# Optimization experiments

Hardware: AMD Instinct MI355X
Metric: run time of the kernel (lower is better)

The kernel has to match this reference:

```python
import jax, jax.numpy as jnp
import numpy as np
from jax.ops import segment_sum

N_NODES = 100000


def _deg_inv_sqrt(idx, n):
    # DGL GraphConv norm='both': degs clamped to min 1, then deg^{-0.5}
    deg = segment_sum(jnp.ones_like(idx, dtype=jnp.float32), idx, num_segments=n)
    return jnp.where(deg > 0, jax.lax.rsqrt(jnp.maximum(deg, 1.0)), 1.0)


def _graph_conv(x, src, dst, W, b, out_norm, in_norm, n):
    # norm='both': scale src feats by out_deg^-1/2, sum-aggregate, scale by in_deg^-1/2
    h = (x * out_norm[:, None]) @ W          # apply weight first (cheaper/equal width)
    msg = h[src]                              # [E, d] irregular gather
    agg = segment_sum(msg, dst, num_segments=n)
    return agg * in_norm[:, None] + b


def setup_inputs() -> dict:
    key = jax.random.key(0)
    k1, k2, k3, k4, k5, k6, k7 = jax.random.split(key, 7)
    E = 1600000
    in_feats, h_feats, out_feats = 128, 128, 64
    in_feat = jax.random.normal(k1, (N_NODES, in_feats), dtype=jnp.float32)
    src = jax.random.randint(k2, (E,), 0, N_NODES, dtype=jnp.int32)
    dst = jax.random.randint(k3, (E,), 0, N_NODES, dtype=jnp.int32)
    # Glorot-style init like dgl GraphConv
    W1 = jax.random.normal(k4, (in_feats, h_feats), dtype=jnp.float32) * (1.0 / np.sqrt(in_feats))
    b1 = jnp.zeros((h_feats,), dtype=jnp.float32)
    W2 = jax.random.normal(k5, (h_feats, out_feats), dtype=jnp.float32) * (1.0 / np.sqrt(h_feats))
    b2 = jnp.zeros((out_feats,), dtype=jnp.float32)
    return {"in_feat": in_feat, "src": src, "dst": dst, "W1": W1, "b1": b1, "W2": W2, "b2": b2}


def reference(in_feat, src, dst, W1, b1, W2, b2):
    n = in_feat.shape[0]
    out_norm = _deg_inv_sqrt(src, n)  # out-degree norm (source side)
    in_norm = _deg_inv_sqrt(dst, n)   # in-degree norm (destination side)
    h = _graph_conv(in_feat, src, dst, W1, b1, out_norm, in_norm, n)
    z = jax.nn.relu(h)
    h2 = _graph_conv(z, src, dst, W2, b2, out_norm, in_norm, n)
    return (h2, z)
```

## Files before the change

### kernel.cpp

```cpp
#include <hip/hip_runtime.h>

#define N_NODES 100000
#define N_EDGES 1600000
#define NB 391
#define BCAP 5120
#define PART_BLOCKS 250
#define EPB 6400
#define GSTRIDE 16

typedef __attribute__((ext_vector_type(8))) short short8;
typedef __attribute__((ext_vector_type(4))) float f32x4;

__device__ inline unsigned short f2bf(float f) {
    unsigned int u = __builtin_bit_cast(unsigned int, f);
    u += 0x7fffu + ((u >> 16) & 1u);
    return (unsigned short)(u >> 16);
}
__device__ inline float bf2f(unsigned short h) {
    unsigned int u = ((unsigned int)h) << 16;
    return __builtin_bit_cast(float, u);
}

__global__ __launch_bounds__(256) void k_part(const int* __restrict__ src, const int* __restrict__ dst,
                                              int* __restrict__ gcurD, int* __restrict__ gcurS,
                                              unsigned int* __restrict__ ebuf,
                                              unsigned char* __restrict__ ebufS,
                                              const float* __restrict__ W1, const float* __restrict__ W2,
                                              unsigned short* __restrict__ Wp1, unsigned short* __restrict__ Wp2) {
    if (blockIdx.x >= PART_BLOCKS) {
        int i = (blockIdx.x - PART_BLOCKS) * 256 + threadIdx.x;
        if (i < 2048) {
            int kq = i >> 7, c = i & 127;
#pragma unroll
            for (int j = 0; j < 8; j++) Wp1[i * 8 + j] = f2bf(W1[(kq * 8 + j) * 128 + c]);
        } else if (i < 3072) {
            int i2 = i - 2048;
            int kq = i2 >> 6, c = i2 & 63;
#pragma unroll
            for (int j = 0; j < 8; j++) Wp2[i2 * 8 + j] = f2bf(W2[(kq * 8 + j) * 64 + c]);
        }
        return;
    }
    __shared__ int histD[NB], gbaseD[NB];
    __shared__ int histS[NB], gbaseS[NB];
    for (int i = threadIdx.x; i < NB; i += 256) { histD[i] = 0; histS[i] = 0; }
    __syncthreads();
    int base = blockIdx.x * EPB;
    for (int i = threadIdx.x; i < EPB; i += 256) {
        int d = dst[base + i], s = src[base + i];
        atomicAdd(&histD[d >> 8], 1);
        atomicAdd(&histS[s >> 8], 1);
    }
    __syncthreads();
    for (int i = threadIdx.x; i < NB; i += 256) {
        int hD = histD[i], hS = histS[i];
        gbaseD[i] = hD ? atomicAdd(&gcurD[i * GSTRIDE], hD) : 0;
        gbaseS[i] = hS ? atomicAdd(&gcurS[i * GSTRIDE], hS) : 0;
        histD[i] = 0;
        histS[i] = 0;
    }
    __syncthreads();
    for (int i = threadIdx.x; i < EPB; i += 256) {
        int d = dst[base + i], s = src[base + i];
        int bd = d >> 8;
        int r = atomicAdd(&histD[bd], 1);
        int pos = gbaseD[bd] + r;
        if (pos < BCAP) ebuf[(size_t)bd * BCAP + pos] = ((unsigned int)s << 8) | (unsigned int)(d & 255);
        int bs = s >> 8;
        int r2 = atomicAdd(&histS[bs], 1);
        int pos2 = gbaseS[bs] + r2;
        if (pos2 < BCAP) ebufS[(size_t)bs * BCAP + pos2] = (unsigned char)(s & 255);
    }
}

__global__ __launch_bounds__(256) void k_bhist_scan(const unsigned char* __restrict__ ebufS,
                                                    const int* __restrict__ gcurS,
                                                    float* __restrict__ out_norm,
                                                    const int* __restrict__ gcurD,
                                                    int* __restrict__ bbase, int* __restrict__ row_ptr) {
    int t = threadIdx.x;
    if (blockIdx.x < NB) {
        __shared__ int hist[256];
        int b = blockIdx.x;
        hist[t] = 0;
        __syncthreads();
        int ne = min(gcurS[b * GSTRIDE], BCAP);
        const unsigned char* eb = ebufS + (size_t)b * BCAP;
        int nv = ne >> 2;
        const uchar4* ev = (const uchar4*)eb;
        for (int i = t; i < nv; i += 256) {
            uchar4 u = ev[i];
            atomicAdd(&hist[u.x], 1); atomicAdd(&hist[u.y], 1);
            atomicAdd(&hist[u.z], 1); atomicAdd(&hist[u.w], 1);
        }
        for (int i = (nv << 2) + t; i < ne; i += 256) atomicAdd(&hist[eb[i]], 1);
        __syncthreads();
        int node = b * 256 + t;
        if (node < N_NODES) out_norm[node] = hist[t] > 0 ? rsqrtf((float)hist[t]) : 1.0f;
    } else {
        __shared__ int s[NB + 1];
        for (int i = t; i < NB; i += 256) s[i] = min(gcurD[i * GSTRIDE], BCAP);
        __syncthreads();
        if (t == 0) {
            int run = 0;
            for (int b = 0; b < NB; b++) { int v = s[b]; s[b] = run; run += v; }
            s[NB] = run;
        }
        __syncthreads();
        for (int i = t; i < NB + 1; i += 256) bbase[i] = s[i];
        if (t == 0) row_ptr[N_NODES] = s[NB];
    }
}

__global__ __launch_bounds__(256) void k_bsort_xb(const unsigned int* __restrict__ ebuf, const int* __restrict__ gcurD,
                                                  const int* __restrict__ bbase, int* __restrict__ csr_src,
                                                  int* __restrict__ row_ptr, float* __restrict__ in_norm,
                                                  const float* __restrict__ x, const float* __restrict__ out_norm,
                                                  unsigned short* __restrict__ xb) {
    __shared__ int perm[BCAP];
    __shared__ int hist[256], cursor[256], sa[256], sb[256];
    int t = threadIdx.x;
    if (blockIdx.x >= NB) {
        int tid = (blockIdx.x - NB) * 256 + t;
        int row = tid >> 5;
        float4 v = ((const float4*)x)[tid];
        float w = out_norm[row];
        unsigned int lo = (unsigned int)f2bf(v.x * w) | ((unsigned int)f2bf(v.y * w) << 16);
        unsigned int hi = (unsigned int)f2bf(v.z * w) | ((unsigned int)f2bf(v.w * w) << 16);
        ((uint2*)xb)[tid] = make_uint2(lo, hi);
        return;
    }
    int b = blockIdx.x;
    int ne = min(gcurD[b * GSTRIDE], BCAP);
    const unsigned int* eb = ebuf + (size_t)b * BCAP;
    hist[t] = 0;
    __syncthreads();
    for (int i = t; i < ne; i += 256) atomicAdd(&hist[eb[i] & 255u], 1);
    __syncthreads();
    sa[t] = hist[t];
    __syncthreads();
    int* cur = sa; int* nxt = sb;
    for (int o = 1; o < 256; o <<= 1) {
        int v = cur[t] + (t >= o ? cur[t - o] : 0);
        nxt[t] = v;
        __syncthreads();
        int* tmp = cur; cur = nxt; nxt = tmp;
    }
    int ex = cur[t] - hist[t];
    cursor[t] = ex;
    int node = b * 256 + t;
    if (node < N_NODES) {
        row_ptr[node] = bbase[b] + ex;
        in_norm[node] = hist[t] > 0 ? rsqrtf((float)hist[t]) : 1.0f;
    }
    __syncthreads();
    for (int i = t; i < ne; i += 256) {
        unsigned int pk = eb[i];
        int pos = atomicAdd(&cursor[pk & 255u], 1);
        perm[pos] = (int)(pk >> 8);
    }
    __syncthreads();
    int gb = bbase[b];
    for (int i = t; i < ne; i += 256) csr_src[gb + i] = perm[i];
}

__global__ __launch_bounds__(256) void k_agg1(const unsigned short* __restrict__ xb,
                                              const int* __restrict__ row_ptr, const int* __restrict__ csr,
                                              const float* __restrict__ in_norm,
                                              unsigned short* __restrict__ aggb) {
    int wave = threadIdx.x >> 6, lane = threadIdx.x & 63;
    int d = blockIdx.x * 4 + wave;
    if (d >= N_NODES) return;
    int e0 = __builtin_amdgcn_readfirstlane(row_ptr[d]);
    int e1 = __builtin_amdgcn_readfirstlane(row_ptr[d + 1]);
    int col = lane << 1;
    float accL[8], accH[8];
#pragma unroll
    for (int j = 0; j < 8; j++) { accL[j] = 0.f; accH[j] = 0.f; }
    int e = e0;
    for (; e + 8 <= e1; e += 8) {
        int sI[8];
#pragma unroll
        for (int j = 0; j < 8; j++) sI[j] = __builtin_amdgcn_readfirstlane(csr[e + j]);
        unsigned int v[8];
#pragma unroll
        for (int j = 0; j < 8; j++) v[j] = *(const unsigned int*)(xb + (size_t)sI[j] * 128 + col);
#pragma unroll
        for (int j = 0; j < 8; j++) {
            accL[j] += bf2f((unsigned short)(v[j] & 0xffffu));
            accH[j] += bf2f((unsigned short)(v[j] >> 16));
        }
    }
    if (e + 4 <= e1) {
        int sI[4];
#pragma unroll
        for (int j = 0; j < 4; j++) sI[j] = __builtin_amdgcn_readfirstlane(csr[e + j]);
        unsigned int v[4];
#pragma unroll
        for (int j = 0; j < 4; j++) v[j] = *(const unsigned int*)(xb + (size_t)sI[j] * 128 + col);
#pragma unroll
        for (int j = 0; j < 4; j++) {
            accL[j] += bf2f((unsigned short)(v[j] & 0xffffu));
            accH[j] += bf2f((unsigned short)(v[j] >> 16));
        }
        e += 4;
    }
    if (e + 2 <= e1) {
        int sI[2];
#pragma unroll
        for (int j = 0; j < 2; j++) sI[j] = __builtin_amdgcn_readfirstlane(csr[e + j]);
        unsigned int v[2];
#pragma unroll
        for (int j = 0; j < 2; j++) v[j] = *(const unsigned int*)(xb + (size_t)sI[j] * 128 + col);
#pragma unroll
        for (int j = 0; j < 2; j++) {
            accL[j] += bf2f((unsigned short)(v[j] & 0xffffu));
            accH[j] += bf2f((unsigned short)(v[j] >> 16));
        }
        e += 2;
    }
    if (e < e1) {
        int s = __builtin_amdgcn_readfirstlane(csr[e]);
        unsigned int v = *(const unsigned int*)(xb + (size_t)s * 128 + col);
        accL[0] += bf2f((unsigned short)(v & 0xffffu));
        accH[0] += bf2f((unsigned short)(v >> 16));
    }
    float a0 = 0.f, a1 = 0.f;
#pragma unroll
    for (int j = 0; j < 8; j++) { a0 += accL[j]; a1 += accH[j]; }
    float w = in_norm[d];
    unsigned int pk = (unsigned int)f2bf(a0 * w) | ((unsigned int)f2bf(a1 * w) << 16);
    *(unsigned int*)(aggb + (size_t)d * 128 + col) = pk;
}

__global__ __launch_bounds__(256) void k_gemm12(const unsigned short* __restrict__ Ab,
                                                const unsigned short* __restrict__ Wp1,
                                                const unsigned short* __restrict__ Wp2,
                                                const float* __restrict__ bias1,
                                                const float* __restrict__ out_norm,
                                                float* __restrict__ z_out,
                                                unsigned short* __restrict__ tb) {
    __shared__ __align__(16) unsigned short lds1[16 * 128 * 8];
    __shared__ __align__(16) unsigned short lds2[16 * 64 * 8];
    __shared__ __align__(16) unsigned short zt[64 * 132];
    {
        const uint4* s1 = (const uint4*)Wp1; uint4* d1 = (uint4*)lds1;
        for (int i = threadIdx.x; i < 2048; i += 256) d1[i] = s1[i];
        const uint4* s2 = (const uint4*)Wp2; uint4* d2 = (uint4*)lds2;
        for (int i = threadIdx.x; i < 1024; i += 256) d2[i] = s2[i];
    }
    __syncthreads();
    int wave = threadIdx.x >> 6, lane = threadIdx.x & 63;
    int base = (blockIdx.x * 4 + wave) * 16;
    if (base >= N_NODES) return;
    int m = lane & 15, q = lane >> 4;
    short8 a[4];
#pragma unroll
    for (int t = 0; t < 4; t++) a[t] = *(const short8*)(Ab + (size_t)(base + m) * 128 + t * 32 + q * 8);
    f32x4 acc[8];
#pragma unroll
    for (int c = 0; c < 8; c++) acc[c] = (f32x4)(0.f);
#pragma unroll
    for (int ct = 0; ct < 8; ct++) {
#pragma unroll
        for (int t = 0; t < 4; t++) {
            short8 b = *(const short8*)(lds1 + ((t * 4 + q) * 128 + ct * 16 + m) * 8);
            acc[ct] = __builtin_amdgcn_mfma_f32_16x16x32_bf16(a[t], b, acc[ct], 0, 0, 0);
        }
    }
    float onr[4];
#pragma unroll
    for (int i = 0; i < 4; i++) onr[i] = out_norm[base + q * 4 + i];
#pragma unroll
    for (int ct = 0; ct < 8; ct++) {
        int col = ct * 16 + m;
        float bv = bias1[col];
#pragma unroll
        for (int i = 0; i < 4; i++) {
            int row = base + q * 4 + i;
            float v = acc[ct][i] + bv;
            v = v > 0.f ? v : 0.f;
            z_out[(size_t)row * 128 + col] = v;
            zt[(wave * 16 + q * 4 + i) * 132 + col] = f2bf(v * onr[i]);
        }
    }
    short8 a2[4];
#pragma unroll
    for (int t = 0; t < 4; t++) a2[t] = *(const short8*)(zt + (wave * 16 + m) * 132 + t * 32 + q * 8);
    f32x4 acc2[4];
#pragma unroll
    for (int c = 0; c < 4; c++) acc2[c] = (f32x4)(0.f);
#pragma unroll
    for (int ct = 0; ct < 4; ct++) {
#pragma unroll
        for (int t = 0; t < 4; t++) {
            short8 b = *(const short8*)(lds2 + ((t * 4 + q) * 64 + ct * 16 + m) * 8);
            acc2[ct] = __builtin_amdgcn_mfma_f32_16x16x32_bf16(a2[t], b, acc2[ct], 0, 0, 0);
        }
    }
#pragma unroll
    for (int ct = 0; ct < 4; ct++) {
        int col = ct * 16 + m;
#pragma unroll
        for (int i = 0; i < 4; i++) {
            int row = base + q * 4 + i;
            tb[(size_t)row * 64 + col] = f2bf(acc2[ct][i]);
        }
    }
}

__global__ __launch_bounds__(256) void k_agg2(const unsigned short* __restrict__ tb,
                                              const int* __restrict__ row_ptr, const int* __restrict__ csr,
                                              const float* __restrict__ in_norm, const float* __restrict__ b2,
                                              float* __restrict__ out_h2) {
    int wave = threadIdx.x >> 6, lane = threadIdx.x & 63;
    int d = blockIdx.x * 4 + wave;
    if (d >= N_NODES) return;
    int e0 = __builtin_amdgcn_readfirstlane(row_ptr[d]);
    int e1 = __builtin_amdgcn_readfirstlane(row_ptr[d + 1]);
    float acc[8];
#pragma unroll
    for (int j = 0; j < 8; j++) acc[j] = 0.f;
    int e = e0;
    for (; e + 8 <= e1; e += 8) {
        int sI[8];
#pragma unroll
        for (int j = 0; j < 8; j++) sI[j] = __builtin_amdgcn_readfirstlane(csr[e + j]);
        unsigned short v[8];
#pragma unroll
        for (int j = 0; j < 8; j++) v[j] = tb[(size_t)sI[j] * 64 + lane];
#pragma unroll
        for (int j = 0; j < 8; j++) acc[j] += bf2f(v[j]);
    }
    if (e + 4 <= e1) {
        int sI[4];
#pragma unroll
        for (int j = 0; j < 4; j++) sI[j] = __builtin_amdgcn_readfirstlane(csr[e + j]);
        unsigned short v[4];
#pragma unroll
        for (int j = 0; j < 4; j++) v[j] = tb[(size_t)sI[j] * 64 + lane];
#pragma unroll
        for (int j = 0; j < 4; j++) acc[j] += bf2f(v[j]);
        e += 4;
    }
    if (e + 2 <= e1) {
        int sI[2];
#pragma unroll
        for (int j = 0; j < 2; j++) sI[j] = __builtin_amdgcn_readfirstlane(csr[e + j]);
        unsigned short v[2];
#pragma unroll
        for (int j = 0; j < 2; j++) v[j] = tb[(size_t)sI[j] * 64 + lane];
#pragma unroll
        for (int j = 0; j < 2; j++) acc[j] += bf2f(v[j]);
        e += 2;
    }
    if (e < e1) {
        int s = __builtin_amdgcn_readfirstlane(csr[e]);
        acc[0] += bf2f(tb[(size_t)s * 64 + lane]);
    }
    float a = 0.f;
#pragma unroll
    for (int j = 0; j < 8; j++) a += acc[j];
    out_h2[(size_t)d * 64 + lane] = a * in_norm[d] + b2[lane];
}

extern "C" void kernel_launch(void* const* d_in, const int* in_sizes, int n_in,
                              void* d_out, int out_size, void* d_ws, size_t ws_size,
                              hipStream_t stream) {
    const float* x   = (const float*)d_in[0];
    const int*   src = (const int*)d_in[1];
    const int*   dst = (const int*)d_in[2];
    const float* W1  = (const float*)d_in[3];
    const float* b1  = (const float*)d_in[4];
    const float* W2  = (const float*)d_in[5];
    const float* b2  = (const float*)d_in[6];
    float* out_h2 = (float*)d_out;
    float* out_z  = (float*)d_out + N_NODES * 64;

    char* ws = (char*)d_ws;
    size_t off = 0;
    auto alloc = [&](size_t bytes) -> char* {
        char* p = ws + off;
        off = (off + bytes + 255) & ~(size_t)255;
        return p;
    };
    int* gcurD    = (int*)alloc(NB * GSTRIDE * 4);
    int* gcurS    = (int*)alloc(NB * GSTRIDE * 4);
    int* bbase    = (int*)alloc((NB + 1) * 4);
    int* row_ptr  = (int*)alloc((N_NODES + 1) * 4);
    float* out_norm = (float*)alloc(N_NODES * 4);
    float* in_norm  = (float*)alloc(N_NODES * 4);
    unsigned int* ebuf = (unsigned int*)alloc((size_t)NB * BCAP * 4);
    unsigned char* ebufS = (unsigned char*)alloc((size_t)NB * BCAP);
    int* csr_src  = (int*)alloc((size_t)N_EDGES * 4);
    unsigned short* Wp1 = (unsigned short*)alloc(2048 * 8 * 2);
    unsigned short* Wp2 = (unsigned short*)alloc(1024 * 8 * 2);
    unsigned short* xb    = (unsigned short*)alloc((size_t)N_NODES * 128 * 2);
    unsigned short* agg1b = (unsigned short*)alloc((size_t)N_NODES * 128 * 2);
    unsigned short* tb    = (unsigned short*)alloc((size_t)N_NODES * 64 * 2);
    (void)ws_size; (void)in_sizes; (void)n_in; (void)out_size;

    hipMemsetAsync(gcurD, 0, NB * GSTRIDE * 4, stream);
    hipMemsetAsync(gcurS, 0, NB * GSTRIDE * 4, stream);

    const int GD_AGG = (N_NODES + 3) / 4;
    const int GD_GEMM = (N_NODES / 16 + 3) / 4;
    const int GD_XB = N_NODES * 32 / 256;

    k_part<<<PART_BLOCKS + 12, 256, 0, stream>>>(src, dst, gcurD, gcurS, ebuf, ebufS, W1, W2, Wp1, Wp2);
    k_bhist_scan<<<NB + 1, 256, 0, stream>>>(ebufS, gcurS, out_norm, gcurD, bbase, row_ptr);
    k_bsort_xb<<<NB + GD_XB, 256, 0, stream>>>(ebuf, gcurD, bbase, csr_src, row_ptr, in_norm, x, out_norm, xb);
    k_agg1<<<GD_AGG, 256, 0, stream>>>(xb, row_ptr, csr_src, in_norm, agg1b);
    k_gemm12<<<GD_GEMM, 256, 0, stream>>>(agg1b, Wp1, Wp2, b1, out_norm, out_z, tb);
    k_agg2<<<GD_AGG, 256, 0, stream>>>(tb, row_ptr, csr_src, in_norm, b2, out_h2);
}
```

Baseline: 300.8 us.

## Replace source-bucket histogram with global atomic degree counts and drop scan kernel

Source out-degrees are now counted with global atomics into a per-node array. This replaces the second bucketing pass into a byte buffer and its per-bucket histogram kernel. The bucket-base prefix scan is folded into the sort kernel, where each block sums the preceding bucket counts itself, so one kernel launch and the byte buffer disappear. The partition kernel also moves to 1024-thread blocks, the two memsets merge into one, and consumers compute rsqrt of the degree inline. The cost is 1.6M contended global atomics and a redundant per-block reduction over up to 391 counts.

```diff
diff --git a/kernel.cpp b/kernel.cpp
--- a/kernel.cpp
+++ b/kernel.cpp
@@ -21,14 +21,13 @@
     return __builtin_bit_cast(float, u);
 }
 
-__global__ __launch_bounds__(256) void k_part(const int* __restrict__ src, const int* __restrict__ dst,
-                                              int* __restrict__ gcurD, int* __restrict__ gcurS,
-                                              unsigned int* __restrict__ ebuf,
-                                              unsigned char* __restrict__ ebufS,
-                                              const float* __restrict__ W1, const float* __restrict__ W2,
-                                              unsigned short* __restrict__ Wp1, unsigned short* __restrict__ Wp2) {
+__global__ __launch_bounds__(1024) void k_part(const int* __restrict__ src, const int* __restrict__ dst,
+                                               int* __restrict__ gcurD, int* __restrict__ degS,
+                                               unsigned int* __restrict__ ebuf,
+                                               const float* __restrict__ W1, const float* __restrict__ W2,
+                                               unsigned short* __restrict__ Wp1, unsigned short* __restrict__ Wp2) {
     if (blockIdx.x >= PART_BLOCKS) {
-        int i = (blockIdx.x - PART_BLOCKS) * 256 + threadIdx.x;
+        int i = (blockIdx.x - PART_BLOCKS) * 1024 + threadIdx.x;
         if (i < 2048) {
             int kq = i >> 7, c = i & 127;
 #pragma unroll
@@ -42,80 +41,35 @@
         return;
     }
     __shared__ int histD[NB], gbaseD[NB];
-    __shared__ int histS[NB], gbaseS[NB];
-    for (int i = threadIdx.x; i < NB; i += 256) { histD[i] = 0; histS[i] = 0; }
+    int t = threadIdx.x;
+    for (int i = t; i < NB; i += 1024) histD[i] = 0;
     __syncthreads();
     int base = blockIdx.x * EPB;
-    for (int i = threadIdx.x; i < EPB; i += 256) {
+    for (int i = t; i < EPB; i += 1024) {
         int d = dst[base + i], s = src[base + i];
         atomicAdd(&histD[d >> 8], 1);
-        atomicAdd(&histS[s >> 8], 1);
-    }
-    __syncthreads();
-    for (int i = threadIdx.x; i < NB; i += 256) {
-        int hD = histD[i], hS = histS[i];
-        gbaseD[i] = hD ? atomicAdd(&gcurD[i * GSTRIDE], hD) : 0;
-        gbaseS[i] = hS ? atomicAdd(&gcurS[i * GSTRIDE], hS) : 0;
+        atomicAdd(&degS[s], 1);
+    }
+    __syncthreads();
+    for (int i = t; i < NB; i += 1024) {
+        int h = histD[i];
+        gbaseD[i] = h ? atomicAdd(&gcurD[i * GSTRIDE], h) : 0;
         histD[i] = 0;
-        histS[i] = 0;
-    }
-    __syncthreads();
-    for (int i = threadIdx.x; i < EPB; i += 256) {
+    }
+    __syncthreads();
+    for (int i = t; i < EPB; i += 1024) {
         int d = dst[base + i], s = src[base + i];
         int bd = d >> 8;
         int r = atomicAdd(&histD[bd], 1);
         int pos = gbaseD[bd] + r;
         if (pos < BCAP) ebuf[(size_t)bd * BCAP + pos] = ((unsigned int)s << 8) | (unsigned int)(d & 255);
-        int bs = s >> 8;
-        int r2 = atomicAdd(&histS[bs], 1);
-        int pos2 = gbaseS[bs] + r2;
-        if (pos2 < BCAP) ebufS[(size_t)bs * BCAP + pos2] = (unsigned char)(s & 255);
-    }
-}
-
-__global__ __launch_bounds__(256) void k_bhist_scan(const unsigned char* __restrict__ ebufS,
-                                                    const int* __restrict__ gcurS,
-                                                    float* __restrict__ out_norm,
-                                                    const int* __restrict__ gcurD,
-                                                    int* __restrict__ bbase, int* __restrict__ row_ptr) {
-    int t = threadIdx.x;
-    if (blockIdx.x < NB) {
-        __shared__ int hist[256];
-        int b = blockIdx.x;
-        hist[t] = 0;
-        __syncthreads();
-        int ne = min(gcurS[b * GSTRIDE], BCAP);
-        const unsigned char* eb = ebufS + (size_t)b * BCAP;
-        int nv = ne >> 2;
-        const uchar4* ev = (const uchar4*)eb;
-        for (int i = t; i < nv; i += 256) {
-            uchar4 u = ev[i];
-            atomicAdd(&hist[u.x], 1); atomicAdd(&hist[u.y], 1);
-            atomicAdd(&hist[u.z], 1); atomicAdd(&hist[u.w], 1);
-        }
-        for (int i = (nv << 2) + t; i < ne; i += 256) atomicAdd(&hist[eb[i]], 1);
-        __syncthreads();
-        int node = b * 256 + t;
-        if (node < N_NODES) out_norm[node] = hist[t] > 0 ? rsqrtf((float)hist[t]) : 1.0f;
-    } else {
-        __shared__ int s[NB + 1];
-        for (int i = t; i < NB; i += 256) s[i] = min(gcurD[i * GSTRIDE], BCAP);
-        __syncthreads();
-        if (t == 0) {
-            int run = 0;
-            for (int b = 0; b < NB; b++) { int v = s[b]; s[b] = run; run += v; }
-            s[NB] = run;
-        }
-        __syncthreads();
-        for (int i = t; i < NB + 1; i += 256) bbase[i] = s[i];
-        if (t == 0) row_ptr[N_NODES] = s[NB];
     }
 }
 
 __global__ __launch_bounds__(256) void k_bsort_xb(const unsigned int* __restrict__ ebuf, const int* __restrict__ gcurD,
-                                                  const int* __restrict__ bbase, int* __restrict__ csr_src,
+                                                  int* __restrict__ csr_src,
                                                   int* __restrict__ row_ptr, float* __restrict__ in_norm,
-                                                  const float* __restrict__ x, const float* __restrict__ out_norm,
+                                                  const float* __restrict__ x, const int* __restrict__ degS,
                                                   unsigned short* __restrict__ xb) {
     __shared__ int perm[BCAP];
     __shared__ int hist[256], cursor[256], sa[256], sb[256];
@@ -124,7 +78,8 @@
         int tid = (blockIdx.x - NB) * 256 + t;
         int row = tid >> 5;
         float4 v = ((const float4*)x)[tid];
-        float w = out_norm[row];
+        int dg = degS[row];
+        float w = dg > 0 ? rsqrtf((float)dg) : 1.0f;
         unsigned int lo = (unsigned int)f2bf(v.x * w) | ((unsigned int)f2bf(v.y * w) << 16);
         unsigned int hi = (unsigned int)f2bf(v.z * w) | ((unsigned int)f2bf(v.w * w) << 16);
         ((uint2*)xb)[tid] = make_uint2(lo, hi);
@@ -133,6 +88,16 @@
     int b = blockIdx.x;
     int ne = min(gcurD[b * GSTRIDE], BCAP);
     const unsigned int* eb = ebuf + (size_t)b * BCAP;
+    int partial = 0;
+    for (int i = t; i < b; i += 256) partial += min(gcurD[i * GSTRIDE], BCAP);
+    sa[t] = partial;
+    __syncthreads();
+    for (int o = 128; o > 0; o >>= 1) {
+        if (t < o) sa[t] += sa[t + o];
+        __syncthreads();
+    }
+    int gb = sa[0];
+    __syncthreads();
     hist[t] = 0;
     __syncthreads();
     for (int i = t; i < ne; i += 256) atomicAdd(&hist[eb[i] & 255u], 1);
@@ -150,9 +115,10 @@
     cursor[t] = ex;
     int node = b * 256 + t;
     if (node < N_NODES) {
-        row_ptr[node] = bbase[b] + ex;
+        row_ptr[node] = gb + ex;
         in_norm[node] = hist[t] > 0 ? rsqrtf((float)hist[t]) : 1.0f;
     }
+    if (b == NB - 1 && t == 0) row_ptr[N_NODES] = gb + ne;
     __syncthreads();
     for (int i = t; i < ne; i += 256) {
         unsigned int pk = eb[i];
@@ -160,7 +126,6 @@
         perm[pos] = (int)(pk >> 8);
     }
     __syncthreads();
-    int gb = bbase[b];
     for (int i = t; i < ne; i += 256) csr_src[gb + i] = perm[i];
 }
 
@@ -237,7 +202,7 @@
                                                 const unsigned short* __restrict__ Wp1,
                                                 const unsigned short* __restrict__ Wp2,
                                                 const float* __restrict__ bias1,
-                                                const float* __restrict__ out_norm,
+                                                const int* __restrict__ degS,
                                                 float* __restrict__ z_out,
                                                 unsigned short* __restrict__ tb) {
     __shared__ __align__(16) unsigned short lds1[16 * 128 * 8];
@@ -270,7 +235,10 @@
     }
     float onr[4];
 #pragma unroll
-    for (int i = 0; i < 4; i++) onr[i] = out_norm[base + q * 4 + i];
+    for (int i = 0; i < 4; i++) {
+        int dg = degS[base + q * 4 + i];
+        onr[i] = dg > 0 ? rsqrtf((float)dg) : 1.0f;
+    }
 #pragma unroll
     for (int ct = 0; ct < 8; ct++) {
         int col = ct * 16 + m;
@@ -385,13 +353,10 @@
         return p;
     };
     int* gcurD    = (int*)alloc(NB * GSTRIDE * 4);
-    int* gcurS    = (int*)alloc(NB * GSTRIDE * 4);
-    int* bbase    = (int*)alloc((NB + 1) * 4);
+    int* degS     = (int*)alloc(N_NODES * 4);
     int* row_ptr  = (int*)alloc((N_NODES + 1) * 4);
-    float* out_norm = (float*)alloc(N_NODES * 4);
     float* in_norm  = (float*)alloc(N_NODES * 4);
     unsigned int* ebuf = (unsigned int*)alloc((size_t)NB * BCAP * 4);
-    unsigned char* ebufS = (unsigned char*)alloc((size_t)NB * BCAP);
     int* csr_src  = (int*)alloc((size_t)N_EDGES * 4);
     unsigned short* Wp1 = (unsigned short*)alloc(2048 * 8 * 2);
     unsigned short* Wp2 = (unsigned short*)alloc(1024 * 8 * 2);
@@ -400,17 +365,16 @@
     unsigned short* tb    = (unsigned short*)alloc((size_t)N_NODES * 64 * 2);
     (void)ws_size; (void)in_sizes; (void)n_in; (void)out_size;
 
-    hipMemsetAsync(gcurD, 0, NB * GSTRIDE * 4, stream);
-    hipMemsetAsync(gcurS, 0, NB * GSTRIDE * 4, stream);
+    const size_t gcur_pad = ((size_t)(NB * GSTRIDE * 4) + 255) & ~(size_t)255;
+    hipMemsetAsync(gcurD, 0, gcur_pad + (size_t)N_NODES * 4, stream);
 
     const int GD_AGG = (N_NODES + 3) / 4;
     const int GD_GEMM = (N_NODES / 16 + 3) / 4;
     const int GD_XB = N_NODES * 32 / 256;
 
-    k_part<<<PART_BLOCKS + 12, 256, 0, stream>>>(src, dst, gcurD, gcurS, ebuf, ebufS, W1, W2, Wp1, Wp2);
-    k_bhist_scan<<<NB + 1, 256, 0, stream>>>(ebufS, gcurS, out_norm, gcurD, bbase, row_ptr);
-    k_bsort_xb<<<NB + GD_XB, 256, 0, stream>>>(ebuf, gcurD, bbase, csr_src, row_ptr, in_norm, x, out_norm, xb);
+    k_part<<<PART_BLOCKS + 3, 1024, 0, stream>>>(src, dst, gcurD, degS, ebuf, W1, W2, Wp1, Wp2);
+    k_bsort_xb<<<NB + GD_XB, 256, 0, stream>>>(ebuf, gcurD, csr_src, row_ptr, in_norm, x, degS, xb);
     k_agg1<<<GD_AGG, 256, 0, stream>>>(xb, row_ptr, csr_src, in_norm, agg1b);
-    k_gemm12<<<GD_GEMM, 256, 0, stream>>>(agg1b, Wp1, Wp2, b1, out_norm, out_z, tb);
+    k_gemm12<<<GD_GEMM, 256, 0, stream>>>(agg1b, Wp1, Wp2, b1, degS, out_z, tb);
     k_agg2<<<GD_AGG, 256, 0, stream>>>(tb, row_ptr, csr_src, in_norm, b2, out_h2);
 }
```

Result: slower. 328.2 us (+9.1%).

## Fuse layer-1 aggregation into the dual-GEMM kernel via per-wave LDS tiles

Applied to the files above, without the earlier changes.

Merges the first gather-aggregation kernel into the GEMM kernel. Each wave now aggregates 16 destination nodes serially, writes them as a bf16 tile in LDS, and feeds that tile straight into the two MFMA GEMMs, so the intermediate agg1 buffer no longer goes through global memory. Weight fragments are now read directly from global memory (cached) instead of being staged into LDS. The cost is much less parallelism: there are 16x fewer waves for the latency-bound gather, and each wave walks its 16 nodes' edge lists one after another, which may hurt latency hiding.

```diff
diff --git a/kernel.cpp b/kernel.cpp
--- a/kernel.cpp
+++ b/kernel.cpp
@@ -164,99 +164,86 @@
     for (int i = t; i < ne; i += 256) csr_src[gb + i] = perm[i];
 }
 
-__global__ __launch_bounds__(256) void k_agg1(const unsigned short* __restrict__ xb,
-                                              const int* __restrict__ row_ptr, const int* __restrict__ csr,
-                                              const float* __restrict__ in_norm,
-                                              unsigned short* __restrict__ aggb) {
-    int wave = threadIdx.x >> 6, lane = threadIdx.x & 63;
-    int d = blockIdx.x * 4 + wave;
-    if (d >= N_NODES) return;
-    int e0 = __builtin_amdgcn_readfirstlane(row_ptr[d]);
-    int e1 = __builtin_amdgcn_readfirstlane(row_ptr[d + 1]);
-    int col = lane << 1;
-    float accL[8], accH[8];
-#pragma unroll
-    for (int j = 0; j < 8; j++) { accL[j] = 0.f; accH[j] = 0.f; }
-    int e = e0;
-    for (; e + 8 <= e1; e += 8) {
-        int sI[8];
-#pragma unroll
-        for (int j = 0; j < 8; j++) sI[j] = __builtin_amdgcn_readfirstlane(csr[e + j]);
-        unsigned int v[8];
-#pragma unroll
-        for (int j = 0; j < 8; j++) v[j] = *(const unsigned int*)(xb + (size_t)sI[j] * 128 + col);
-#pragma unroll
-        for (int j = 0; j < 8; j++) {
-            accL[j] += bf2f((unsigned short)(v[j] & 0xffffu));
-            accH[j] += bf2f((unsigned short)(v[j] >> 16));
-        }
-    }
-    if (e + 4 <= e1) {
-        int sI[4];
-#pragma unroll
-        for (int j = 0; j < 4; j++) sI[j] = __builtin_amdgcn_readfirstlane(csr[e + j]);
-        unsigned int v[4];
-#pragma unroll
-        for (int j = 0; j < 4; j++) v[j] = *(const unsigned int*)(xb + (size_t)sI[j] * 128 + col);
-#pragma unroll
-        for (int j = 0; j < 4; j++) {
-            accL[j] += bf2f((unsigned short)(v[j] & 0xffffu));
-            accH[j] += bf2f((unsigned short)(v[j] >> 16));
-        }
-        e += 4;
-    }
-    if (e + 2 <= e1) {
-        int sI[2];
-#pragma unroll
-        for (int j = 0; j < 2; j++) sI[j] = __builtin_amdgcn_readfirstlane(csr[e + j]);
-        unsigned int v[2];
-#pragma unroll
-        for (int j = 0; j < 2; j++) v[j] = *(const unsigned int*)(xb + (size_t)sI[j] * 128 + col);
-#pragma unroll
-        for (int j = 0; j < 2; j++) {
-            accL[j] += bf2f((unsigned short)(v[j] & 0xffffu));
-            accH[j] += bf2f((unsigned short)(v[j] >> 16));
-        }
-        e += 2;
-    }
-    if (e < e1) {
-        int s = __builtin_amdgcn_readfirstlane(csr[e]);
-        unsigned int v = *(const unsigned int*)(xb + (size_t)s * 128 + col);
-        accL[0] += bf2f((unsigned short)(v & 0xffffu));
-        accH[0] += bf2f((unsigned short)(v >> 16));
-    }
-    float a0 = 0.f, a1 = 0.f;
-#pragma unroll
-    for (int j = 0; j < 8; j++) { a0 += accL[j]; a1 += accH[j]; }
-    float w = in_norm[d];
-    unsigned int pk = (unsigned int)f2bf(a0 * w) | ((unsigned int)f2bf(a1 * w) << 16);
-    *(unsigned int*)(aggb + (size_t)d * 128 + col) = pk;
-}
-
-__global__ __launch_bounds__(256) void k_gemm12(const unsigned short* __restrict__ Ab,
-                                                const unsigned short* __restrict__ Wp1,
-                                                const unsigned short* __restrict__ Wp2,
-                                                const float* __restrict__ bias1,
-                                                const float* __restrict__ out_norm,
-                                                float* __restrict__ z_out,
-                                                unsigned short* __restrict__ tb) {
-    __shared__ __align__(16) unsigned short lds1[16 * 128 * 8];
-    __shared__ __align__(16) unsigned short lds2[16 * 64 * 8];
-    __shared__ __align__(16) unsigned short zt[64 * 132];
-    {
-        const uint4* s1 = (const uint4*)Wp1; uint4* d1 = (uint4*)lds1;
-        for (int i = threadIdx.x; i < 2048; i += 256) d1[i] = s1[i];
-        const uint4* s2 = (const uint4*)Wp2; uint4* d2 = (uint4*)lds2;
-        for (int i = threadIdx.x; i < 1024; i += 256) d2[i] = s2[i];
-    }
-    __syncthreads();
+__global__ __launch_bounds__(256) void k_agg1g(const unsigned short* __restrict__ xb,
+                                               const int* __restrict__ row_ptr, const int* __restrict__ csr,
+                                               const float* __restrict__ in_norm, const float* __restrict__ out_norm,
+                                               const unsigned short* __restrict__ Wp1,
+                                               const unsigned short* __restrict__ Wp2,
+                                               const float* __restrict__ bias1,
+                                               float* __restrict__ z_out, unsigned short* __restrict__ tb) {
+    __shared__ __align__(16) unsigned short zt[4][16 * 132];
     int wave = threadIdx.x >> 6, lane = threadIdx.x & 63;
     int base = (blockIdx.x * 4 + wave) * 16;
     if (base >= N_NODES) return;
+    unsigned short* zw = &zt[wave][0];
+    int col = lane << 1;
+#pragma unroll 1
+    for (int i = 0; i < 16; i++) {
+        int d = base + i;
+        int e0 = __builtin_amdgcn_readfirstlane(row_ptr[d]);
+        int e1 = __builtin_amdgcn_readfirstlane(row_ptr[d + 1]);
+        float accL[8], accH[8];
+#pragma unroll
+        for (int j = 0; j < 8; j++) { accL[j] = 0.f; accH[j] = 0.f; }
+        int e = e0;
+        for (; e + 8 <= e1; e += 8) {
+            int sI[8];
+#pragma unroll
+            for (int j = 0; j < 8; j++) sI[j] = __builtin_amdgcn_readfirstlane(csr[e + j]);
+            unsigned int v[8];
+#pragma unroll
+            for (int j = 0; j < 8; j++) v[j] = *(const unsigned int*)(xb + (size_t)sI[j] * 128 + col);
+#pragma unroll
+            for (int j = 0; j < 8; j++) {
+                accL[j] += bf2f((unsigned short)(v[j] & 0xffffu));
+                accH[j] += bf2f((unsigned short)(v[j] >> 16));
+            }
+        }
+        if (e + 4 <= e1) {
+            int sI[4];
+#pragma unroll
+            for (int j = 0; j < 4; j++) sI[j] = __builtin_amdgcn_readfirstlane(csr[e + j]);
+            unsigned int v[4];
+#pragma unroll
+            for (int j = 0; j < 4; j++) v[j] = *(const unsigned int*)(xb + (size_t)sI[j] * 128 + col);
+#pragma unroll
+            for (int j = 0; j < 4; j++) {
+                accL[j] += bf2f((unsigned short)(v[j] & 0xffffu));
+                accH[j] += bf2f((unsigned short)(v[j] >> 16));
+            }
+            e += 4;
+        }
+        if (e + 2 <= e1) {
+            int sI[2];
+#pragma unroll
+            for (int j = 0; j < 2; j++) sI[j] = __builtin_amdgcn_readfirstlane(csr[e + j]);
+            unsigned int v[2];
+#pragma unroll
+            for (int j = 0; j < 2; j++) v[j] = *(const unsigned int*)(xb + (size_t)sI[j] * 128 + col);
+#pragma unroll
+            for (int j = 0; j < 2; j++) {
+                accL[j] += bf2f((unsigned short)(v[j] & 0xffffu));
+                accH[j] += bf2f((unsigned short)(v[j] >> 16));
+            }
+            e += 2;
+        }
+        if (e < e1) {
+            int s = __builtin_amdgcn_readfirstlane(csr[e]);
+            unsigned int v = *(const unsigned int*)(xb + (size_t)s * 128 + col);
+            accL[0] += bf2f((unsigned short)(v & 0xffffu));
+            accH[0] += bf2f((unsigned short)(v >> 16));
+        }
+        float a0 = 0.f, a1 = 0.f;
+#pragma unroll
+        for (int j = 0; j < 8; j++) { a0 += accL[j]; a1 += accH[j]; }
+        float w = in_norm[d];
+        unsigned int pk = (unsigned int)f2bf(a0 * w) | ((unsigned int)f2bf(a1 * w) << 16);
+        *(unsigned int*)(zw + i * 132 + col) = pk;
+    }
     int m = lane & 15, q = lane >> 4;
     short8 a[4];
 #pragma unroll
-    for (int t = 0; t < 4; t++) a[t] = *(const short8*)(Ab + (size_t)(base + m) * 128 + t * 32 + q * 8);
+    for (int t = 0; t < 4; t++) a[t] = *(const short8*)(zw + m * 132 + t * 32 + q * 8);
     f32x4 acc[8];
 #pragma unroll
     for (int c = 0; c < 8; c++) acc[c] = (f32x4)(0.f);
@@ -264,7 +251,7 @@
     for (int ct = 0; ct < 8; ct++) {
 #pragma unroll
         for (int t = 0; t < 4; t++) {
-            short8 b = *(const short8*)(lds1 + ((t * 4 + q) * 128 + ct * 16 + m) * 8);
+            short8 b = *(const short8*)(Wp1 + ((size_t)((t * 4 + q) * 128 + ct * 16 + m)) * 8);
             acc[ct] = __builtin_amdgcn_mfma_f32_16x16x32_bf16(a[t], b, acc[ct], 0, 0, 0);
         }
     }
@@ -273,20 +260,20 @@
     for (int i = 0; i < 4; i++) onr[i] = out_norm[base + q * 4 + i];
 #pragma unroll
     for (int ct = 0; ct < 8; ct++) {
-        int col = ct * 16 + m;
-        float bv = bias1[col];
+        int c2 = ct * 16 + m;
+        float bv = bias1[c2];
 #pragma unroll
         for (int i = 0; i < 4; i++) {
             int row = base + q * 4 + i;
             float v = acc[ct][i] + bv;
             v = v > 0.f ? v : 0.f;
-            z_out[(size_t)row * 128 + col] = v;
-            zt[(wave * 16 + q * 4 + i) * 132 + col] = f2bf(v * onr[i]);
+            z_out[(size_t)row * 128 + c2] = v;
+            zw[(q * 4 + i) * 132 + c2] = f2bf(v * onr[i]);
         }
     }
     short8 a2[4];
 #pragma unroll
-    for (int t = 0; t < 4; t++) a2[t] = *(const short8*)(zt + (wave * 16 + m) * 132 + t * 32 + q * 8);
+    for (int t = 0; t < 4; t++) a2[t] = *(const short8*)(zw + m * 132 + t * 32 + q * 8);
     f32x4 acc2[4];
 #pragma unroll
     for (int c = 0; c < 4; c++) acc2[c] = (f32x4)(0.f);
@@ -294,17 +281,17 @@
     for (int ct = 0; ct < 4; ct++) {
 #pragma unroll
         for (int t = 0; t < 4; t++) {
-            short8 b = *(const short8*)(lds2 + ((t * 4 + q) * 64 + ct * 16 + m) * 8);
+            short8 b = *(const short8*)(Wp2 + ((size_t)((t * 4 + q) * 64 + ct * 16 + m)) * 8);
             acc2[ct] = __builtin_amdgcn_mfma_f32_16x16x32_bf16(a2[t], b, acc2[ct], 0, 0, 0);
         }
     }
 #pragma unroll
     for (int ct = 0; ct < 4; ct++) {
-        int col = ct * 16 + m;
+        int c2 = ct * 16 + m;
 #pragma unroll
         for (int i = 0; i < 4; i++) {
             int row = base + q * 4 + i;
-            tb[(size_t)row * 64 + col] = f2bf(acc2[ct][i]);
+            tb[(size_t)row * 64 + c2] = f2bf(acc2[ct][i]);
         }
     }
 }
@@ -396,7 +383,6 @@
     unsigned short* Wp1 = (unsigned short*)alloc(2048 * 8 * 2);
     unsigned short* Wp2 = (unsigned short*)alloc(1024 * 8 * 2);
     unsigned short* xb    = (unsigned short*)alloc((size_t)N_NODES * 128 * 2);
-    unsigned short* agg1b = (unsigned short*)alloc((size_t)N_NODES * 128 * 2);
     unsigned short* tb    = (unsigned short*)alloc((size_t)N_NODES * 64 * 2);
     (void)ws_size; (void)in_sizes; (void)n_in; (void)out_size;
 
@@ -404,13 +390,12 @@
     hipMemsetAsync(gcurS, 0, NB * GSTRIDE * 4, stream);
 
     const int GD_AGG = (N_NODES + 3) / 4;
-    const int GD_GEMM = (N_NODES / 16 + 3) / 4;
-    const int GD_XB = N_NODES * 32 / 256;
+    const int GD_F   = (N_NODES / 16 + 3) / 4;
+    const int GD_XB  = N_NODES * 32 / 256;
 
     k_part<<<PART_BLOCKS + 12, 256, 0, stream>>>(src, dst, gcurD, gcurS, ebuf, ebufS, W1, W2, Wp1, Wp2);
     k_bhist_scan<<<NB + 1, 256, 0, stream>>>(ebufS, gcurS, out_norm, gcurD, bbase, row_ptr);
     k_bsort_xb<<<NB + GD_XB, 256, 0, stream>>>(ebuf, gcurD, bbase, csr_src, row_ptr, in_norm, x, out_norm, xb);
-    k_agg1<<<GD_AGG, 256, 0, stream>>>(xb, row_ptr, csr_src, in_norm, agg1b);
-    k_gemm12<<<GD_GEMM, 256, 0, stream>>>(agg1b, Wp1, Wp2, b1, out_norm, out_z, tb);
+    k_agg1g<<<GD_F, 256, 0, stream>>>(xb, row_ptr, csr_src, in_norm, out_norm, Wp1, Wp2, b1, out_z, tb);
     k_agg2<<<GD_AGG, 256, 0, stream>>>(tb, row_ptr, csr_src, in_norm, b2, out_h2);
 }
```

Result: no change. 306.4 us (+1.9%).
